# Performance work log

Measured on AMD Instinct MI355X. Metric: run time of the kernel, lower is better.

Reference implementation:

```python
import jax, jax.numpy as jnp
import numpy as np

COORD_DIM = 4
HIDDEN = 256
N_HIDDEN_LAYERS = 4  # num_layers - 1 hidden->hidden layers after the first
MIN_OMEGA = 10.0
MAX_OMEGA = 100.0
MEDIAN_OMEGA = (MIN_OMEGA + MAX_OMEGA) / 2.0
N = 524288


def _uniform(key, shape, bound):
    return jax.random.uniform(key, shape, jnp.float32, -bound, bound)


def setup_inputs() -> dict:
    key = jax.random.key(0)
    ks = jax.random.split(key, 16)
    coords = jax.random.normal(ks[0], (N, COORD_DIM), jnp.float32)
    # omega predictor: Linear(4, 64) -> ReLU -> Linear(64, 1) -> Sigmoid
    ow1 = _uniform(ks[1], (COORD_DIM, HIDDEN // 4), 1.0 / np.sqrt(COORD_DIM))
    ob1 = _uniform(ks[2], (HIDDEN // 4,), 1.0 / np.sqrt(COORD_DIM))
    ow2 = _uniform(ks[3], (HIDDEN // 4, 1), 1.0 / np.sqrt(HIDDEN // 4))
    ob2 = _uniform(ks[4], (1,), 1.0 / np.sqrt(HIDDEN // 4))
    # SIREN first layer: uniform(-1/in_features, 1/in_features)
    w0 = _uniform(ks[5], (COORD_DIM, HIDDEN), 1.0 / COORD_DIM)
    b0 = _uniform(ks[6], (HIDDEN,), 1.0 / np.sqrt(COORD_DIM))
    # SIREN hidden layers: uniform(-sqrt(6/in)/omega0, ...), stacked [4, 256, 256]
    hb = np.sqrt(6.0 / HIDDEN) / MEDIAN_OMEGA
    wh = _uniform(ks[7], (N_HIDDEN_LAYERS, HIDDEN, HIDDEN), hb)
    bh = _uniform(ks[8], (N_HIDDEN_LAYERS, HIDDEN), 1.0 / np.sqrt(HIDDEN))
    wf = _uniform(ks[9], (HIDDEN, 1), hb)
    bf = _uniform(ks[10], (1,), 1.0 / np.sqrt(HIDDEN))
    return {"coords": coords, "ow1": ow1, "ob1": ob1, "ow2": ow2, "ob2": ob2,
            "w0": w0, "b0": b0, "wh": wh, "bh": bh, "wf": wf, "bf": bf}


def reference(coords, ow1, ob1, ow2, ob2, w0, b0, wh, bh, wf, bf):
    # adaptive omega per coordinate: [N, 1]
    h = jax.nn.relu(coords @ ow1 + ob1)
    omega = MIN_OMEGA + (MAX_OMEGA - MIN_OMEGA) * jax.nn.sigmoid(h @ ow2 + ob2)
    # SIREN stack: x = sin(omega * (x @ W + b))
    x = jnp.sin(omega * (coords @ w0 + b0))
    for i in range(N_HIDDEN_LAYERS):
        x = jnp.sin(omega * (x @ wh[i] + bh[i]))
    return x @ wf + bf  # [N, 1]
```

## Files before the change

### kernel.cpp

```cpp
#include <hip/hip_runtime.h>
#include <hip/hip_bf16.h>

typedef _Float16 f16;
typedef f16 f16x4 __attribute__((ext_vector_type(4)));
typedef f16 f16x8 __attribute__((ext_vector_type(8)));
typedef __fp16 h16x2 __attribute__((ext_vector_type(2)));
typedef __fp16 h16x4 __attribute__((ext_vector_type(4)));
typedef float f32x4 __attribute__((ext_vector_type(4)));
typedef float f32x16 __attribute__((ext_vector_type(16)));

#define MT 128
#define LDST 260
#define INV2PI 0.15915494309189535f

__global__ __launch_bounds__(64)
void prep_wt(const float* __restrict__ wh, f16* __restrict__ wt) {
    const int b = blockIdx.x;
    const int layer = b >> 7, wcblk = (b >> 4) & 7, kblk = b & 15;
    const int lane = threadIdx.x;
    const int l31 = lane & 31, lh = lane >> 5;
    const float* src = wh + layer * 65536 + (kblk * 16 + lh * 8) * 256 + wcblk * 32 + l31;
    f16x8 v;
#pragma unroll
    for (int j = 0; j < 8; j++) v[j] = (f16)src[j * 256];
    *(f16x8*)(wt + b * 512 + lane * 8) = v;
}

__device__ inline f16x8 lds_ld8(const f16* p) {
    f16x4 lo = *(const f16x4*)p;
    f16x4 hi = *(const f16x4*)(p + 4);
    return __builtin_shufflevector(lo, hi, 0, 1, 2, 3, 4, 5, 6, 7);
}

__device__ inline f16x4 pk4(float z0, float z1, float z2, float z3) {
    h16x2 a = __builtin_amdgcn_cvt_pkrtz(z0, z1);
    h16x2 b = __builtin_amdgcn_cvt_pkrtz(z2, z3);
    h16x4 r = __builtin_shufflevector(a, b, 0, 1, 2, 3);
    return __builtin_bit_cast(f16x4, r);
}

__global__ __launch_bounds__(512, 4)
void siren_fused(const float* __restrict__ coords,
                 const float* __restrict__ ow1, const float* __restrict__ ob1,
                 const float* __restrict__ ow2, const float* __restrict__ ob2,
                 const float* __restrict__ w0, const float* __restrict__ b0,
                 const f16* __restrict__ wt,
                 const float* __restrict__ bh,
                 const float* __restrict__ wf,
                 const float* __restrict__ bf,
                 float* __restrict__ out) {
    __shared__ __align__(16) f16 Xs[MT * LDST];
    __shared__ float om_rev[MT];
    __shared__ __align__(16) float crd[MT * 4];
    __shared__ __align__(16) float bh_s[256];
    __shared__ __align__(16) float wf_s[256];

    const int t = threadIdx.x;
    const long base_pt = (long)blockIdx.x * MT;

    if (t < MT) ((f32x4*)crd)[t] = ((const f32x4*)(coords + base_pt * 4))[t];
    if (t < 256) wf_s[t] = wf[t];
    __syncthreads();

    if (t < MT) {
        const float c0 = crd[t * 4], c1 = crd[t * 4 + 1], c2 = crd[t * 4 + 2], c3 = crd[t * 4 + 3];
        float h[64];
#pragma unroll
        for (int j = 0; j < 64; j++) {
            float z = ob1[j] + c0 * ow1[j] + c1 * ow1[64 + j] + c2 * ow1[128 + j] + c3 * ow1[192 + j];
            h[j] = fmaxf(z, 0.f);
        }
        float z2 = ob2[0];
#pragma unroll
        for (int j = 0; j < 64; j++) z2 += h[j] * ow2[j];
        const float sig = 1.f / (1.f + __expf(-z2));
        om_rev[t] = (10.f + 90.f * sig) * INV2PI;
    }
    __syncthreads();

    {
        const int pt = t >> 2;
        const int q = t & 3;
        const float c0 = crd[pt * 4], c1 = crd[pt * 4 + 1], c2 = crd[pt * 4 + 2], c3 = crd[pt * 4 + 3];
        const float orv = om_rev[pt];
#pragma unroll
        for (int i = 0; i < 4; i++) {
            const int ch = (q + 4 * i) * 16;
#pragma unroll
            for (int c = 0; c < 16; c += 4) {
                f32x4 wv0 = *(const f32x4*)(w0 + 0 * 256 + ch + c);
                f32x4 wv1 = *(const f32x4*)(w0 + 1 * 256 + ch + c);
                f32x4 wv2 = *(const f32x4*)(w0 + 2 * 256 + ch + c);
                f32x4 wv3 = *(const f32x4*)(w0 + 3 * 256 + ch + c);
                f32x4 bv  = *(const f32x4*)(b0 + ch + c);
                float z[4];
#pragma unroll
                for (int j = 0; j < 4; j++) {
                    float zz = bv[j] + c0 * wv0[j] + c1 * wv1[j] + c2 * wv2[j] + c3 * wv3[j];
                    z[j] = __builtin_amdgcn_sinf(orv * zz);
                }
                *(f16x4*)&Xs[pt * LDST + ch + c] = pk4(z[0], z[1], z[2], z[3]);
            }
        }
    }
    __syncthreads();

    const int lane = t & 63;
    const int wave = t >> 6;
    const int l31 = lane & 31;
    const int lh = lane >> 5;
    const int wcg = wave & 3;
    const int pr0 = (wave >> 2) * 64;
    const int wc0 = wcg * 64;

    for (int layer = 0; layer < 4; layer++) {
        if (t < 256) bh_s[t] = bh[layer * 256 + t];

        const f16* afrag = wt + ((layer * 8 + wcg * 2) * 16) * 512 + lane * 8;
        const f16* bptr = &Xs[(pr0 + l31) * LDST + lh * 8];

        f32x16 acc[2][2];
#pragma unroll
        for (int ct = 0; ct < 2; ct++)
#pragma unroll
            for (int rt = 0; rt < 2; rt++)
#pragma unroll
                for (int j = 0; j < 16; j++) acc[ct][rt][j] = 0.f;

        f16x8 a0[3], a1[3];
#pragma unroll
        for (int d = 0; d < 3; d++) {
            a0[d] = *(const f16x8*)(afrag + d * 512);
            a1[d] = *(const f16x8*)(afrag + 8192 + d * 512);
        }

#pragma unroll
        for (int kb = 0; kb < 16; kb++) {
            const int s = kb % 3;
            f16x8 av0 = a0[s], av1 = a1[s];
            if (kb + 3 < 16) {
                a0[s] = *(const f16x8*)(afrag + (kb + 3) * 512);
                a1[s] = *(const f16x8*)(afrag + 8192 + (kb + 3) * 512);
            }
            f16x8 bv0 = lds_ld8(bptr + 0 * 32 * LDST + kb * 16);
            f16x8 bv1 = lds_ld8(bptr + 1 * 32 * LDST + kb * 16);
            acc[0][0] = __builtin_amdgcn_mfma_f32_32x32x16_f16(av0, bv0, acc[0][0], 0, 0, 0);
            acc[0][1] = __builtin_amdgcn_mfma_f32_32x32x16_f16(av0, bv1, acc[0][1], 0, 0, 0);
            acc[1][0] = __builtin_amdgcn_mfma_f32_32x32x16_f16(av1, bv0, acc[1][0], 0, 0, 0);
            acc[1][1] = __builtin_amdgcn_mfma_f32_32x32x16_f16(av1, bv1, acc[1][1], 0, 0, 0);
        }
        __syncthreads();

        float orv[2];
#pragma unroll
        for (int rt = 0; rt < 2; rt++) orv[rt] = om_rev[pr0 + rt * 32 + l31];
#pragma unroll
        for (int ct = 0; ct < 2; ct++) {
#pragma unroll
            for (int g = 0; g < 4; g++) {
                const int wc = wc0 + ct * 32 + g * 8 + lh * 4;
                f32x4 bb = *(const f32x4*)&bh_s[wc];
#pragma unroll
                for (int rt = 0; rt < 2; rt++) {
                    const int prow = pr0 + rt * 32 + l31;
                    float z[4];
#pragma unroll
                    for (int j = 0; j < 4; j++)
                        z[j] = __builtin_amdgcn_sinf(orv[rt] * (acc[ct][rt][g * 4 + j] + bb[j]));
                    *(f16x4*)&Xs[prow * LDST + wc] = pk4(z[0], z[1], z[2], z[3]);
                }
            }
        }
        __syncthreads();
    }

    {
        const int pt = t >> 2;
        const int q = t & 3;
        const f16* xrow = &Xs[pt * LDST];
        float s = 0.f;
#pragma unroll
        for (int i = 0; i < 4; i++) {
            const int ch = (q + 4 * i) * 16;
#pragma unroll
            for (int c = 0; c < 16; c += 4) {
                f16x4 xv = *(const f16x4*)(xrow + ch + c);
                f32x4 wv = *(const f32x4*)&wf_s[ch + c];
                s += (float)xv[0] * wv[0] + (float)xv[1] * wv[1]
                   + (float)xv[2] * wv[2] + (float)xv[3] * wv[3];
            }
        }
        s += __shfl_xor(s, 1, 64);
        s += __shfl_xor(s, 2, 64);
        if (q == 0) out[base_pt + pt] = s + bf[0];
    }
}

extern "C" void kernel_launch(void* const* d_in, const int* in_sizes, int n_in,
                              void* d_out, int out_size, void* d_ws, size_t ws_size,
                              hipStream_t stream) {
    (void)in_sizes; (void)n_in; (void)out_size; (void)ws_size;
    const float* coords = (const float*)d_in[0];
    const float* ow1 = (const float*)d_in[1];
    const float* ob1 = (const float*)d_in[2];
    const float* ow2 = (const float*)d_in[3];
    const float* ob2 = (const float*)d_in[4];
    const float* w0  = (const float*)d_in[5];
    const float* b0  = (const float*)d_in[6];
    const float* wh  = (const float*)d_in[7];
    const float* bh  = (const float*)d_in[8];
    const float* wf  = (const float*)d_in[9];
    const float* bf  = (const float*)d_in[10];
    float* out = (float*)d_out;
    f16* wt = (f16*)d_ws;

    prep_wt<<<512, 64, 0, stream>>>(wh, wt);
    siren_fused<<<524288 / MT, 512, 0, stream>>>(coords, ow1, ob1, ow2, ob2,
                                                 w0, b0, wt, bh, wf, bf, out);
}
```

Measured before the change: 442.9 us.

## Double-buffer activations, halve tile to 64 points, fold bias into accumulators

```diff
diff --git a/kernel.cpp b/kernel.cpp
--- a/kernel.cpp
+++ b/kernel.cpp
@@ -9,7 +9,7 @@
 typedef float f32x4 __attribute__((ext_vector_type(4)));
 typedef float f32x16 __attribute__((ext_vector_type(16)));
 
-#define MT 128
+#define MT 64
 #define LDST 260
 #define INV2PI 0.15915494309189535f
 
@@ -39,7 +39,7 @@
     return __builtin_bit_cast(f16x4, r);
 }
 
-__global__ __launch_bounds__(512, 4)
+__global__ __launch_bounds__(256, 2)
 void siren_fused(const float* __restrict__ coords,
                  const float* __restrict__ ow1, const float* __restrict__ ob1,
                  const float* __restrict__ ow2, const float* __restrict__ ob2,
@@ -49,17 +49,16 @@
                  const float* __restrict__ wf,
                  const float* __restrict__ bf,
                  float* __restrict__ out) {
-    __shared__ __align__(16) f16 Xs[MT * LDST];
+    __shared__ __align__(16) f16 Xs[2][MT * LDST];
     __shared__ float om_rev[MT];
     __shared__ __align__(16) float crd[MT * 4];
-    __shared__ __align__(16) float bh_s[256];
     __shared__ __align__(16) float wf_s[256];
 
     const int t = threadIdx.x;
     const long base_pt = (long)blockIdx.x * MT;
 
     if (t < MT) ((f32x4*)crd)[t] = ((const f32x4*)(coords + base_pt * 4))[t];
-    if (t < 256) wf_s[t] = wf[t];
+    wf_s[t] = wf[t];
     __syncthreads();
 
     if (t < MT) {
@@ -99,7 +98,7 @@
                     float zz = bv[j] + c0 * wv0[j] + c1 * wv1[j] + c2 * wv2[j] + c3 * wv3[j];
                     z[j] = __builtin_amdgcn_sinf(orv * zz);
                 }
-                *(f16x4*)&Xs[pt * LDST + ch + c] = pk4(z[0], z[1], z[2], z[3]);
+                *(f16x4*)&Xs[0][pt * LDST + ch + c] = pk4(z[0], z[1], z[2], z[3]);
             }
         }
     }
@@ -109,23 +108,26 @@
     const int wave = t >> 6;
     const int l31 = lane & 31;
     const int lh = lane >> 5;
-    const int wcg = wave & 3;
-    const int pr0 = (wave >> 2) * 64;
-    const int wc0 = wcg * 64;
+    const int wc0 = wave * 64;
 
     for (int layer = 0; layer < 4; layer++) {
-        if (t < 256) bh_s[t] = bh[layer * 256 + t];
-
-        const f16* afrag = wt + ((layer * 8 + wcg * 2) * 16) * 512 + lane * 8;
-        const f16* bptr = &Xs[(pr0 + l31) * LDST + lh * 8];
+        const int cur = layer & 1;
+
+        const f16* afrag = wt + ((layer * 8 + wave * 2) * 16) * 512 + lane * 8;
+        const f16* bptr = &Xs[cur][l31 * LDST + lh * 8];
 
         f32x16 acc[2][2];
 #pragma unroll
         for (int ct = 0; ct < 2; ct++)
 #pragma unroll
-            for (int rt = 0; rt < 2; rt++)
-#pragma unroll
-                for (int j = 0; j < 16; j++) acc[ct][rt][j] = 0.f;
+            for (int g = 0; g < 4; g++) {
+                f32x4 bb = *(const f32x4*)(bh + layer * 256 + wc0 + ct * 32 + g * 8 + lh * 4);
+#pragma unroll
+                for (int j = 0; j < 4; j++) {
+                    acc[ct][0][g * 4 + j] = bb[j];
+                    acc[ct][1][g * 4 + j] = bb[j];
+                }
+            }
 
         f16x8 a0[3], a1[3];
 #pragma unroll
@@ -133,6 +135,8 @@
             a0[d] = *(const f16x8*)(afrag + d * 512);
             a1[d] = *(const f16x8*)(afrag + 8192 + d * 512);
         }
+        f16x8 bv0 = lds_ld8(bptr);
+        f16x8 bv1 = lds_ld8(bptr + 32 * LDST);
 
 #pragma unroll
         for (int kb = 0; kb < 16; kb++) {
@@ -142,32 +146,33 @@
                 a0[s] = *(const f16x8*)(afrag + (kb + 3) * 512);
                 a1[s] = *(const f16x8*)(afrag + 8192 + (kb + 3) * 512);
             }
-            f16x8 bv0 = lds_ld8(bptr + 0 * 32 * LDST + kb * 16);
-            f16x8 bv1 = lds_ld8(bptr + 1 * 32 * LDST + kb * 16);
-            acc[0][0] = __builtin_amdgcn_mfma_f32_32x32x16_f16(av0, bv0, acc[0][0], 0, 0, 0);
-            acc[0][1] = __builtin_amdgcn_mfma_f32_32x32x16_f16(av0, bv1, acc[0][1], 0, 0, 0);
-            acc[1][0] = __builtin_amdgcn_mfma_f32_32x32x16_f16(av1, bv0, acc[1][0], 0, 0, 0);
-            acc[1][1] = __builtin_amdgcn_mfma_f32_32x32x16_f16(av1, bv1, acc[1][1], 0, 0, 0);
-        }
-        __syncthreads();
+            f16x8 b0v = bv0, b1v = bv1;
+            if (kb + 1 < 16) {
+                bv0 = lds_ld8(bptr + (kb + 1) * 16);
+                bv1 = lds_ld8(bptr + 32 * LDST + (kb + 1) * 16);
+            }
+            acc[0][0] = __builtin_amdgcn_mfma_f32_32x32x16_f16(av0, b0v, acc[0][0], 0, 0, 0);
+            acc[0][1] = __builtin_amdgcn_mfma_f32_32x32x16_f16(av0, b1v, acc[0][1], 0, 0, 0);
+            acc[1][0] = __builtin_amdgcn_mfma_f32_32x32x16_f16(av1, b0v, acc[1][0], 0, 0, 0);
+            acc[1][1] = __builtin_amdgcn_mfma_f32_32x32x16_f16(av1, b1v, acc[1][1], 0, 0, 0);
+        }
 
         float orv[2];
-#pragma unroll
-        for (int rt = 0; rt < 2; rt++) orv[rt] = om_rev[pr0 + rt * 32 + l31];
+        orv[0] = om_rev[l31];
+        orv[1] = om_rev[32 + l31];
 #pragma unroll
         for (int ct = 0; ct < 2; ct++) {
 #pragma unroll
             for (int g = 0; g < 4; g++) {
                 const int wc = wc0 + ct * 32 + g * 8 + lh * 4;
-                f32x4 bb = *(const f32x4*)&bh_s[wc];
 #pragma unroll
                 for (int rt = 0; rt < 2; rt++) {
-                    const int prow = pr0 + rt * 32 + l31;
+                    const int prow = rt * 32 + l31;
                     float z[4];
 #pragma unroll
                     for (int j = 0; j < 4; j++)
-                        z[j] = __builtin_amdgcn_sinf(orv[rt] * (acc[ct][rt][g * 4 + j] + bb[j]));
-                    *(f16x4*)&Xs[prow * LDST + wc] = pk4(z[0], z[1], z[2], z[3]);
+                        z[j] = __builtin_amdgcn_sinf(orv[rt] * acc[ct][rt][g * 4 + j]);
+                    *(f16x4*)&Xs[cur ^ 1][prow * LDST + wc] = pk4(z[0], z[1], z[2], z[3]);
                 }
             }
         }
@@ -177,7 +182,7 @@
     {
         const int pt = t >> 2;
         const int q = t & 3;
-        const f16* xrow = &Xs[pt * LDST];
+        const f16* xrow = &Xs[0][pt * LDST];
         float s = 0.f;
 #pragma unroll
         for (int i = 0; i < 4; i++) {
@@ -215,6 +220,6 @@
     f16* wt = (f16*)d_ws;
 
     prep_wt<<<512, 64, 0, stream>>>(wh, wt);
-    siren_fused<<<524288 / MT, 512, 0, stream>>>(coords, ow1, ob1, ow2, ob2,
+    siren_fused<<<524288 / MT, 256, 0, stream>>>(coords, ow1, ob1, ow2, ob2,
                                                  w0, b0, wt, bh, wf, bf, out);
 }
```

Result: slower. 506.3 us (+14.3%).

## Remap waves to 32-column strips over all rows and preload bias into accumulators

Applied to the files above, without the earlier changes.

```diff
diff --git a/kernel.cpp b/kernel.cpp
--- a/kernel.cpp
+++ b/kernel.cpp
@@ -52,7 +52,6 @@
     __shared__ __align__(16) f16 Xs[MT * LDST];
     __shared__ float om_rev[MT];
     __shared__ __align__(16) float crd[MT * 4];
-    __shared__ __align__(16) float bh_s[256];
     __shared__ __align__(16) float wf_s[256];
 
     const int t = threadIdx.x;
@@ -109,66 +108,58 @@
     const int wave = t >> 6;
     const int l31 = lane & 31;
     const int lh = lane >> 5;
-    const int wcg = wave & 3;
-    const int pr0 = (wave >> 2) * 64;
-    const int wc0 = wcg * 64;
-
+    const int wc0 = wave * 32;
+
+#pragma unroll 1
     for (int layer = 0; layer < 4; layer++) {
-        if (t < 256) bh_s[t] = bh[layer * 256 + t];
-
-        const f16* afrag = wt + ((layer * 8 + wcg * 2) * 16) * 512 + lane * 8;
-        const f16* bptr = &Xs[(pr0 + l31) * LDST + lh * 8];
-
-        f32x16 acc[2][2];
-#pragma unroll
-        for (int ct = 0; ct < 2; ct++)
-#pragma unroll
-            for (int rt = 0; rt < 2; rt++)
-#pragma unroll
-                for (int j = 0; j < 16; j++) acc[ct][rt][j] = 0.f;
-
-        f16x8 a0[3], a1[3];
-#pragma unroll
-        for (int d = 0; d < 3; d++) {
-            a0[d] = *(const f16x8*)(afrag + d * 512);
-            a1[d] = *(const f16x8*)(afrag + 8192 + d * 512);
-        }
-
-#pragma unroll
+        const f16* afrag = wt + ((layer * 8 + wave) * 16) * 512 + lane * 8;
+        const f16* bptr = &Xs[l31 * LDST + lh * 8];
+
+        f32x16 acc[4];
+#pragma unroll
+        for (int g = 0; g < 4; g++) {
+            f32x4 bb = *(const f32x4*)(bh + layer * 256 + wc0 + g * 8 + lh * 4);
+#pragma unroll
+            for (int r = 0; r < 4; r++)
+#pragma unroll
+                for (int j = 0; j < 4; j++) acc[r][g * 4 + j] = bb[j];
+        }
+
+        f16x8 a[2];
+        a[0] = *(const f16x8*)(afrag);
+        a[1] = *(const f16x8*)(afrag + 512);
+
+#pragma unroll 4
         for (int kb = 0; kb < 16; kb++) {
-            const int s = kb % 3;
-            f16x8 av0 = a0[s], av1 = a1[s];
-            if (kb + 3 < 16) {
-                a0[s] = *(const f16x8*)(afrag + (kb + 3) * 512);
-                a1[s] = *(const f16x8*)(afrag + 8192 + (kb + 3) * 512);
-            }
+            const int s = kb & 1;
+            f16x8 av = a[s];
+            if (kb + 2 < 16)
+                a[s] = *(const f16x8*)(afrag + (kb + 2) * 512);
             f16x8 bv0 = lds_ld8(bptr + 0 * 32 * LDST + kb * 16);
             f16x8 bv1 = lds_ld8(bptr + 1 * 32 * LDST + kb * 16);
-            acc[0][0] = __builtin_amdgcn_mfma_f32_32x32x16_f16(av0, bv0, acc[0][0], 0, 0, 0);
-            acc[0][1] = __builtin_amdgcn_mfma_f32_32x32x16_f16(av0, bv1, acc[0][1], 0, 0, 0);
-            acc[1][0] = __builtin_amdgcn_mfma_f32_32x32x16_f16(av1, bv0, acc[1][0], 0, 0, 0);
-            acc[1][1] = __builtin_amdgcn_mfma_f32_32x32x16_f16(av1, bv1, acc[1][1], 0, 0, 0);
+            f16x8 bv2 = lds_ld8(bptr + 2 * 32 * LDST + kb * 16);
+            f16x8 bv3 = lds_ld8(bptr + 3 * 32 * LDST + kb * 16);
+            acc[0] = __builtin_amdgcn_mfma_f32_32x32x16_f16(av, bv0, acc[0], 0, 0, 0);
+            acc[1] = __builtin_amdgcn_mfma_f32_32x32x16_f16(av, bv1, acc[1], 0, 0, 0);
+            acc[2] = __builtin_amdgcn_mfma_f32_32x32x16_f16(av, bv2, acc[2], 0, 0, 0);
+            acc[3] = __builtin_amdgcn_mfma_f32_32x32x16_f16(av, bv3, acc[3], 0, 0, 0);
         }
         __syncthreads();
 
-        float orv[2];
-#pragma unroll
-        for (int rt = 0; rt < 2; rt++) orv[rt] = om_rev[pr0 + rt * 32 + l31];
-#pragma unroll
-        for (int ct = 0; ct < 2; ct++) {
-#pragma unroll
-            for (int g = 0; g < 4; g++) {
-                const int wc = wc0 + ct * 32 + g * 8 + lh * 4;
-                f32x4 bb = *(const f32x4*)&bh_s[wc];
-#pragma unroll
-                for (int rt = 0; rt < 2; rt++) {
-                    const int prow = pr0 + rt * 32 + l31;
-                    float z[4];
-#pragma unroll
-                    for (int j = 0; j < 4; j++)
-                        z[j] = __builtin_amdgcn_sinf(orv[rt] * (acc[ct][rt][g * 4 + j] + bb[j]));
-                    *(f16x4*)&Xs[prow * LDST + wc] = pk4(z[0], z[1], z[2], z[3]);
-                }
+        float orv[4];
+#pragma unroll
+        for (int r = 0; r < 4; r++) orv[r] = om_rev[r * 32 + l31];
+#pragma unroll
+        for (int g = 0; g < 4; g++) {
+            const int wc = wc0 + g * 8 + lh * 4;
+#pragma unroll
+            for (int r = 0; r < 4; r++) {
+                const int prow = r * 32 + l31;
+                float z[4];
+#pragma unroll
+                for (int j = 0; j < 4; j++)
+                    z[j] = __builtin_amdgcn_sinf(orv[r] * acc[r][g * 4 + j]);
+                *(f16x4*)&Xs[prow * LDST + wc] = pk4(z[0], z[1], z[2], z[3]);
             }
         }
         __syncthreads();
```

Result: no change. 446.0 us (+0.7%).
